# Optimization experiments

Hardware: AMD Instinct MI355X
Metric: run time of the kernel (lower is better)

## Reference

```python
import jax, jax.numpy as jnp
import numpy as np

B, T, C = 2, 2048, 1024
H = 16
HD = C // H  # 64


def setup_inputs() -> dict:
    key = jax.random.key(0)
    ks = jax.random.split(key, 6)
    s_in = 1.0 / np.sqrt(C)
    s_pr = 1.0 / np.sqrt(H * HD)
    x = jax.random.normal(ks[0], (B, T, C), dtype=jnp.float32)
    Wq = jax.random.uniform(ks[1], (H, C, HD), jnp.float32, -s_in, s_in)
    Wk = jax.random.uniform(ks[2], (H, C, HD), jnp.float32, -s_in, s_in)
    Wv = jax.random.uniform(ks[3], (H, C, HD), jnp.float32, -s_in, s_in)
    Wp = jax.random.uniform(ks[4], (H * HD, C), jnp.float32, -s_pr, s_pr)
    bp = jax.random.uniform(ks[5], (C,), jnp.float32, -s_pr, s_pr)
    return {"x": x, "Wq": Wq, "Wk": Wk, "Wv": Wv, "Wp": Wp, "bp": bp}


def reference(x, Wq, Wk, Wv, Wp, bp):
    # per-head projections: [B,T,C] x [H,C,D] -> [B,H,T,D]
    q = jnp.einsum('btc,hcd->bhtd', x, Wq)
    k = jnp.einsum('btc,hcd->bhtd', x, Wk)
    v = jnp.einsum('btc,hcd->bhtd', x, Wv)
    scale = HD ** (-0.5)
    scores = jnp.einsum('bhtd,bhsd->bhts', q, k) * scale  # [B,H,T,T]
    causal = jnp.tril(jnp.ones((T, T), dtype=bool))
    scores = jnp.where(causal, scores, -jnp.inf)
    w = jax.nn.softmax(scores, axis=-1)
    out = jnp.einsum('bhts,bhsd->bhtd', w, v)  # [B,H,T,D]
    # concat heads: [B,T,H*D] (head order matches torch.cat over heads)
    out = jnp.transpose(out, (0, 2, 1, 3)).reshape(B, T, H * HD)
    return out @ Wp + bp
```

## Files before the change

### kernel.cpp

```cpp
#include <hip/hip_runtime.h>
#include <hip/hip_bf16.h>
#include <hip/hip_cooperative_groups.h>

namespace cg = cooperative_groups;

#define B_NUM 2
#define T_SEQ 2048
#define C_DIM 1024
#define H_NUM 16
#define HD    64
#define M_TOT 4096
#define BH_N  32

typedef __attribute__((ext_vector_type(8))) short short8;
typedef __attribute__((ext_vector_type(4))) float floatx4;

__device__ __forceinline__ short f2bf(float f) {
    unsigned u = __float_as_uint(f);
    u += 0x7FFFu + ((u >> 16) & 1u);
    return (short)(u >> 16);
}

__device__ __forceinline__ unsigned pk2bf(float a, float b) {
    float2 f2; f2.x = a; f2.y = b;
    __hip_bfloat162 h = __float22bfloat162_rn(f2);
    unsigned u; __builtin_memcpy(&u, &h, 4); return u;
}

__device__ __forceinline__ void gld16(const short* g, short* l) {
    __builtin_amdgcn_global_load_lds(
        (const __attribute__((address_space(1))) void*)g,
        (__attribute__((address_space(3))) void*)l, 16, 0, 0);
}

__global__ __launch_bounds__(512, 2) void mega(
    const float* __restrict__ x,  const float* __restrict__ Wq,
    const float* __restrict__ Wk, const float* __restrict__ Wv,
    const float* __restrict__ Wp, const float* __restrict__ bp,
    short* __restrict__ xb, short* __restrict__ wt, short* __restrict__ wpt,
    short* __restrict__ qb, short* __restrict__ kb, short* __restrict__ vtb,
    short* __restrict__ attb, float* __restrict__ out) {

    __shared__ short smem[26112];
    cg::grid_group grid = cg::this_grid();

    const int G   = gridDim.x;
    const int bid = blockIdx.x;
    const int tid = threadIdx.x;
    const int lane = tid & 63, w = tid >> 6;
    const int hi = lane >> 4, llo = lane & 15;
    const int lrow = lane >> 3;
    const int lswz = ((lane & 7) ^ (lrow & 7)) * 8;
    const int fc0 = (hi ^ (llo & 7)) * 8;
    const int fc1 = ((hi + 4) ^ (llo & 7)) * 8;

    {
        int gtid = bid * 512 + tid;
        for (int i = gtid; i < 524288; i += G * 512) {
            int idx = i * 8;
            float4 a = *(const float4*)(x + idx);
            float4 b4 = *(const float4*)(x + idx + 4);
            short8 o;
            o[0] = f2bf(a.x);  o[1] = f2bf(a.y);  o[2] = f2bf(a.z);  o[3] = f2bf(a.w);
            o[4] = f2bf(b4.x); o[5] = f2bf(b4.y); o[6] = f2bf(b4.z); o[7] = f2bf(b4.w);
            *(short8*)(xb + idx) = o;
        }
        short (*sh)[72] = (short(*)[72])smem;
        for (int unit = bid; unit < 1024; unit += G) {
            __syncthreads();
            if (unit < 768) {
                const int y = unit >> 4, ct = unit & 15;
                const int which = y >> 4, h = y & 15;
                const float* W = ((which == 0) ? Wq : (which == 1) ? Wk : Wv)
                                 + (size_t)h * C_DIM * HD;
                const int c0 = ct * 64;
                #pragma unroll
                for (int p = 0; p < 2; ++p) {
                    int idx = tid + 512 * p;
                    int c = idx >> 4, d4 = idx & 15;
                    float4 v = *(const float4*)(W + (size_t)(c0 + c) * HD + d4 * 4);
                    sh[d4 * 4 + 0][c] = f2bf(v.x);
                    sh[d4 * 4 + 1][c] = f2bf(v.y);
                    sh[d4 * 4 + 2][c] = f2bf(v.z);
                    sh[d4 * 4 + 3][c] = f2bf(v.w);
                }
                __syncthreads();
                int d = tid >> 3, cc = tid & 7;
                short8 vv = *(const short8*)(&sh[d][cc * 8]);
                *(short8*)(wt + ((size_t)(which * 16 + h) * 64 + d) * C_DIM + c0 + cc * 8) = vv;
            } else {
                const int u2 = unit - 768;
                const int nt = u2 >> 4, ct = u2 & 15;
                #pragma unroll
                for (int p = 0; p < 2; ++p) {
                    int idx = tid + 512 * p;
                    int k = idx >> 4, n4 = idx & 15;
                    float4 v = *(const float4*)(Wp + (size_t)(ct * 64 + k) * C_DIM + nt * 64 + n4 * 4);
                    sh[n4 * 4 + 0][k] = f2bf(v.x);
                    sh[n4 * 4 + 1][k] = f2bf(v.y);
                    sh[n4 * 4 + 2][k] = f2bf(v.z);
                    sh[n4 * 4 + 3][k] = f2bf(v.w);
                }
                __syncthreads();
                int n = tid >> 3, cc = tid & 7;
                short8 vv = *(const short8*)(&sh[n][cc * 8]);
                *(short8*)(wpt + (size_t)(nt * 64 + n) * C_DIM + ct * 64 + cc * 8) = vv;
            }
        }
    }
    grid.sync();

    for (int tile = bid; tile < 512; tile += G) {
        const int mt = tile >> 4, ntg = tile & 15;
        const int m0 = mt * 128, n0 = ntg * 192;
        const int wm = w & 1, wn = w >> 1;
        short* As = smem;
        short* Bs = smem + 8192;

        floatx4 acc[4][3];
        #pragma unroll
        for (int i = 0; i < 4; ++i)
            #pragma unroll
            for (int j = 0; j < 3; ++j)
                #pragma unroll
                for (int r = 0; r < 4; ++r) acc[i][j][r] = 0.0f;

        const size_t a_base = (size_t)(m0 + w * 16 + lrow) * C_DIM + lswz;
        const size_t b_base = (size_t)(n0 + w * 24 + lrow) * C_DIM + lswz;

        for (int kt = 0; kt < C_DIM / 64; ++kt) {
            const int c0 = kt * 64;
            __syncthreads();
            #pragma unroll
            for (int p = 0; p < 2; ++p)
                gld16(xb + a_base + (size_t)p * 8 * C_DIM + c0, &As[(w * 16 + p * 8) * 64]);
            #pragma unroll
            for (int p = 0; p < 3; ++p)
                gld16(wt + b_base + (size_t)p * 8 * C_DIM + c0, &Bs[(w * 24 + p * 8) * 64]);
            __syncthreads();

            short8 af[4][2];
            #pragma unroll
            for (int mi = 0; mi < 4; ++mi) {
                const int row = wm * 64 + mi * 16 + llo;
                af[mi][0] = *(const short8*)(&As[row * 64 + fc0]);
                af[mi][1] = *(const short8*)(&As[row * 64 + fc1]);
            }
            #pragma unroll
            for (int ni = 0; ni < 3; ++ni) {
                const int row = wn * 48 + ni * 16 + llo;
                short8 b0 = *(const short8*)(&Bs[row * 64 + fc0]);
                short8 b1 = *(const short8*)(&Bs[row * 64 + fc1]);
                #pragma unroll
                for (int mi = 0; mi < 4; ++mi) {
                    acc[mi][ni] = __builtin_amdgcn_mfma_f32_16x16x32_bf16(af[mi][0], b0, acc[mi][ni], 0, 0, 0);
                    acc[mi][ni] = __builtin_amdgcn_mfma_f32_16x16x32_bf16(af[mi][1], b1, acc[mi][ni], 0, 0, 0);
                }
            }
        }

        const int bb = m0 >> 11;
        #pragma unroll
        for (int c = 0; c < 3; ++c) {
            const int n_chunk = n0 + 64 * c;
            const int which = n_chunk >> 10;
            const int h = (n_chunk >> 6) & 15;
            __syncthreads();
            if (which == 2) {
                short (*R)[136] = (short(*)[136])smem;
                #pragma unroll
                for (int ni = 0; ni < 3; ++ni) {
                    const int gcol = wn * 48 + ni * 16;
                    if ((gcol >> 6) == c) {
                        #pragma unroll
                        for (int mi = 0; mi < 4; ++mi)
                            #pragma unroll
                            for (int r = 0; r < 4; ++r)
                                R[(gcol & 63) + llo][wm * 64 + mi * 16 + hi * 4 + r] =
                                    f2bf(acc[mi][ni][r]);
                    }
                }
                __syncthreads();
                #pragma unroll
                for (int p = 0; p < 2; ++p) {
                    int idx = tid + 512 * p;
                    int rr = idx >> 4, cc = idx & 15;
                    short8 vv = *(const short8*)(&R[rr][cc * 8]);
                    int t = (m0 & 2047) + cc * 8;
                    *(short8*)(vtb + ((size_t)((bb * H_NUM + h) * HD + rr)) * T_SEQ + t) = vv;
                }
            } else {
                short (*R)[72] = (short(*)[72])smem;
                const float scl = (which == 0) ? 0.125f * 1.4426950408889634f : 1.0f;
                #pragma unroll
                for (int ni = 0; ni < 3; ++ni) {
                    const int gcol = wn * 48 + ni * 16;
                    if ((gcol >> 6) == c) {
                        #pragma unroll
                        for (int mi = 0; mi < 4; ++mi)
                            #pragma unroll
                            for (int r = 0; r < 4; ++r)
                                R[wm * 64 + mi * 16 + hi * 4 + r][(gcol & 63) + llo] =
                                    f2bf(acc[mi][ni][r] * scl);
                    }
                }
                __syncthreads();
                short* outp = (which == 0) ? qb : kb;
                #pragma unroll
                for (int p = 0; p < 2; ++p) {
                    int idx = tid + 512 * p;
                    int r = idx >> 3, cc = idx & 7;
                    short8 vv = *(const short8*)(&R[r][cc * 8]);
                    int t = (m0 + r) & 2047;
                    *(short8*)(outp + ((size_t)(bb * H_NUM + h) * T_SEQ + t) * HD + cc * 8) = vv;
                }
            }
        }
    }
    grid.sync();

    for (int unit = bid; unit < 512; unit += G) {
        const int bh = unit & 31;
        const int y = unit >> 5;
        const int qt = (y < 8) ? (15 - y) : (y - 8);
        const int b = bh >> 4, h = bh & 15;
        const short* K  = kb  + (size_t)bh * T_SEQ * HD;
        const short* Vt = vtb + (size_t)bh * HD * T_SEQ;

        short* Ks = smem;
        short* Vs = smem + 8192;
        short (*Ps)[76] = (short(*)[76])(smem + 16384);

        const int kmax = 2 * qt + 1;

        short8 qf[2];
        const int qcol0 = qt * 128 + w * 16;
        #pragma unroll
        for (int kh = 0; kh < 2; ++kh)
            qf[kh] = *(const short8*)(qb +
                ((size_t)bh * T_SEQ + qcol0 + llo) * HD + kh * 32 + hi * 8);

        short8 av4;
        #pragma unroll
        for (int j = 0; j < 8; ++j) av4[j] = (llo == 0) ? (short)0x3F80 : (short)0;

        gld16(K + (size_t)(w * 8 + lrow) * HD + lswz, &Ks[(w * 8) * 64]);
        gld16(Vt + (size_t)(w * 8 + lrow) * T_SEQ + lswz, &Vs[(w * 8) * 64]);

        floatx4 Oa[5];
        #pragma unroll
        for (int n = 0; n < 5; ++n)
            #pragma unroll
            for (int r = 0; r < 4; ++r) Oa[n][r] = 0.0f;

        for (int kt = 0; kt <= kmax; ++kt) {
            __syncthreads();
            const int buf = (kt & 1) * 4096;

            if (kt + 1 <= kmax) {
                const int s0 = (kt + 1) * 64;
                const int nb = ((kt + 1) & 1) * 4096;
                gld16(K + ((size_t)s0 + w * 8 + lrow) * HD + lswz, &Ks[nb + (w * 8) * 64]);
                gld16(Vt + (size_t)(w * 8 + lrow) * T_SEQ + s0 + lswz, &Vs[nb + (w * 8) * 64]);
            }

            short8 ak[4][2];
            #pragma unroll
            for (int nt = 0; nt < 4; ++nt) {
                const int row = nt * 16 + llo;
                ak[nt][0] = *(const short8*)(&Ks[buf + row * 64 + fc0]);
                ak[nt][1] = *(const short8*)(&Ks[buf + row * 64 + fc1]);
            }
            floatx4 sf[4];
            #pragma unroll
            for (int nt = 0; nt < 4; ++nt)
                #pragma unroll
                for (int r = 0; r < 4; ++r) sf[nt][r] = 0.0f;
            #pragma unroll
            for (int nt = 0; nt < 4; ++nt)
                #pragma unroll
                for (int kh = 0; kh < 2; ++kh)
                    sf[nt] = __builtin_amdgcn_mfma_f32_16x16x32_bf16(
                        ak[nt][kh], qf[kh], sf[nt], 0, 0, 0);

            const int sbase = kt * 64;
            if (sbase + 63 > qcol0) {
                const int qlane = qcol0 + llo;
                #pragma unroll
                for (int nt = 0; nt < 4; ++nt)
                    #pragma unroll
                    for (int r = 0; r < 4; ++r)
                        if (sbase + nt * 16 + hi * 4 + r > qlane) sf[nt][r] = -3.0e38f;
            }

            #pragma unroll
            for (int nt = 0; nt < 4; ++nt) {
                float p0 = __builtin_amdgcn_exp2f(sf[nt][0]);
                float p1 = __builtin_amdgcn_exp2f(sf[nt][1]);
                float p2 = __builtin_amdgcn_exp2f(sf[nt][2]);
                float p3 = __builtin_amdgcn_exp2f(sf[nt][3]);
                uint2 u; u.x = pk2bf(p0, p1); u.y = pk2bf(p2, p3);
                *(uint2*)(&Ps[w * 16 + llo][nt * 16 + hi * 4]) = u;
            }

            short8 av[5][2];
            #pragma unroll
            for (int nt2 = 0; nt2 < 4; ++nt2) {
                const int row = nt2 * 16 + llo;
                av[nt2][0] = *(const short8*)(&Vs[buf + row * 64 + fc0]);
                av[nt2][1] = *(const short8*)(&Vs[buf + row * 64 + fc1]);
            }
            av[4][0] = av4;
            av[4][1] = av4;
            short8 bpf[2];
            #pragma unroll
            for (int kh = 0; kh < 2; ++kh)
                bpf[kh] = *(const short8*)(&Ps[w * 16 + llo][kh * 32 + hi * 8]);
            #pragma unroll
            for (int nt2 = 0; nt2 < 5; ++nt2)
                #pragma unroll
                for (int kh = 0; kh < 2; ++kh)
                    Oa[nt2] = __builtin_amdgcn_mfma_f32_16x16x32_bf16(
                        av[nt2][kh], bpf[kh], Oa[nt2], 0, 0, 0);
        }

        {
            float lb = __shfl(Oa[4][0], llo);
            float inv = 1.0f / lb;
            #pragma unroll
            for (int nt2 = 0; nt2 < 4; ++nt2) {
                uint2 u;
                u.x = pk2bf(Oa[nt2][0] * inv, Oa[nt2][1] * inv);
                u.y = pk2bf(Oa[nt2][2] * inv, Oa[nt2][3] * inv);
                *(uint2*)(&Ps[w * 16 + llo][nt2 * 16 + hi * 4]) = u;
            }
        }
        __syncthreads();
        #pragma unroll
        for (int p = 0; p < 2; ++p) {
            int idx = tid + 512 * p;
            int r = idx >> 3, cc = idx & 7;
            short8 vv = *(const short8*)(&Ps[r][cc * 8]);
            *(short8*)(attb + ((size_t)(b * T_SEQ + qt * 128 + r)) * C_DIM + h * HD + cc * 8) = vv;
        }
        __syncthreads();
    }
    grid.sync();

    for (int tile = bid; tile < 512; tile += G) {
        const int mt = tile >> 4, ntg = tile & 15;
        const int m0 = mt * 128, n0 = ntg * 64;
        const int wm = w & 1, wn = w >> 1;
        short* As = smem;
        short* Bs = smem + 8192;

        floatx4 acc[4];
        #pragma unroll
        for (int i = 0; i < 4; ++i)
            #pragma unroll
            for (int r = 0; r < 4; ++r) acc[i][r] = 0.0f;

        const size_t a_base = (size_t)(m0 + w * 16 + lrow) * C_DIM + lswz;
        const size_t b_base = (size_t)(n0 + w * 8 + lrow) * C_DIM + lswz;

        for (int kt = 0; kt < C_DIM / 64; ++kt) {
            const int c0 = kt * 64;
            __syncthreads();
            #pragma unroll
            for (int p = 0; p < 2; ++p)
                gld16(attb + a_base + (size_t)p * 8 * C_DIM + c0, &As[(w * 16 + p * 8) * 64]);
            gld16(wpt + b_base + c0, &Bs[(w * 8) * 64]);
            __syncthreads();

            short8 af[4][2];
            #pragma unroll
            for (int mi = 0; mi < 4; ++mi) {
                const int row = wm * 64 + mi * 16 + llo;
                af[mi][0] = *(const short8*)(&As[row * 64 + fc0]);
                af[mi][1] = *(const short8*)(&As[row * 64 + fc1]);
            }
            const int brow = wn * 16 + llo;
            short8 b0 = *(const short8*)(&Bs[brow * 64 + fc0]);
            short8 b1 = *(const short8*)(&Bs[brow * 64 + fc1]);
            #pragma unroll
            for (int mi = 0; mi < 4; ++mi) {
                acc[mi] = __builtin_amdgcn_mfma_f32_16x16x32_bf16(af[mi][0], b0, acc[mi], 0, 0, 0);
                acc[mi] = __builtin_amdgcn_mfma_f32_16x16x32_bf16(af[mi][1], b1, acc[mi], 0, 0, 0);
            }
        }

        const int n = n0 + wn * 16 + llo;
        const float bias = bp[n];
        #pragma unroll
        for (int mi = 0; mi < 4; ++mi)
            #pragma unroll
            for (int r = 0; r < 4; ++r) {
                int m = m0 + wm * 64 + mi * 16 + hi * 4 + r;
                out[(size_t)m * C_DIM + n] = acc[mi][r] + bias;
            }
        __syncthreads();
    }
}

__global__ __launch_bounds__(256) void prep_k(
    const float* __restrict__ x, const float* __restrict__ Wq,
    const float* __restrict__ Wk, const float* __restrict__ Wv,
    const float* __restrict__ Wp,
    short* __restrict__ xb, short* __restrict__ wt, short* __restrict__ wpt) {
    const int bid = blockIdx.x;
    const int tid = threadIdx.x;
    if (bid < 2048) {
        int idx = (bid * 256 + tid) * 8;
        float4 a = *(const float4*)(x + idx);
        float4 b = *(const float4*)(x + idx + 4);
        short8 o;
        o[0] = f2bf(a.x); o[1] = f2bf(a.y); o[2] = f2bf(a.z); o[3] = f2bf(a.w);
        o[4] = f2bf(b.x); o[5] = f2bf(b.y); o[6] = f2bf(b.z); o[7] = f2bf(b.w);
        *(short8*)(xb + idx) = o;
        return;
    }
    const int b2 = bid - 2048;
    const int ct = b2 & 15, y = b2 >> 4;
    __shared__ short sh[64][72];
    if (y < 48) {
        const int which = y >> 4, h = y & 15;
        const float* W = ((which == 0) ? Wq : (which == 1) ? Wk : Wv) + (size_t)h * C_DIM * HD;
        const int c0 = ct * 64;
        #pragma unroll
        for (int p = 0; p < 4; ++p) {
            int idx = tid + 256 * p;
            int c = idx >> 4, d4 = idx & 15;
            float4 v = *(const float4*)(W + (size_t)(c0 + c) * HD + d4 * 4);
            sh[d4 * 4 + 0][c] = f2bf(v.x);
            sh[d4 * 4 + 1][c] = f2bf(v.y);
            sh[d4 * 4 + 2][c] = f2bf(v.z);
            sh[d4 * 4 + 3][c] = f2bf(v.w);
        }
        __syncthreads();
        #pragma unroll
        for (int p = 0; p < 2; ++p) {
            int idx = tid + 256 * p;
            int d = idx >> 3, cc = idx & 7;
            short8 vv = *(const short8*)(&sh[d][cc * 8]);
            *(short8*)(wt + ((size_t)(which * 16 + h) * 64 + d) * C_DIM + c0 + cc * 8) = vv;
        }
    } else {
        const int nt = y - 48;
        #pragma unroll
        for (int p = 0; p < 4; ++p) {
            int idx = tid + 256 * p;
            int k = idx >> 4, n4 = idx & 15;
            float4 v = *(const float4*)(Wp + (size_t)(ct * 64 + k) * C_DIM + nt * 64 + n4 * 4);
            sh[n4 * 4 + 0][k] = f2bf(v.x);
            sh[n4 * 4 + 1][k] = f2bf(v.y);
            sh[n4 * 4 + 2][k] = f2bf(v.z);
            sh[n4 * 4 + 3][k] = f2bf(v.w);
        }
        __syncthreads();
        #pragma unroll
        for (int p = 0; p < 2; ++p) {
            int idx = tid + 256 * p;
            int n = idx >> 3, cc = idx & 7;
            short8 vv = *(const short8*)(&sh[n][cc * 8]);
            *(short8*)(wpt + (size_t)(nt * 64 + n) * C_DIM + ct * 64 + cc * 8) = vv;
        }
    }
}

__global__ __launch_bounds__(256) void qkv_k(
    const short* __restrict__ xb, const short* __restrict__ wt,
    short* __restrict__ qb, short* __restrict__ kb, short* __restrict__ vtb) {
    const int mt = blockIdx.x, ntg = blockIdx.y;
    const int m0 = mt * 128, n0 = ntg * 128;
    const int which = ntg >> 3;
    const float sc = (which == 0) ? 0.125f * 1.4426950408889634f : 1.0f;

    __shared__ short smem[17408];
    short* As = smem;
    short* Bs = smem + 8192;

    const int tid = threadIdx.x;
    const int lane = tid & 63, w = tid >> 6;
    const int wm = w & 1, wn = w >> 1;
    const int hi = lane >> 4, llo = lane & 15;
    const int lrow = lane >> 3;
    const int lswz = ((lane & 7) ^ (lrow & 7)) * 8;
    const int fc0 = (hi ^ (llo & 7)) * 8;
    const int fc1 = ((hi + 4) ^ (llo & 7)) * 8;

    floatx4 acc[4][4];
    #pragma unroll
    for (int i = 0; i < 4; ++i)
        #pragma unroll
        for (int j = 0; j < 4; ++j)
            #pragma unroll
            for (int r = 0; r < 4; ++r) acc[i][j][r] = 0.0f;

    const size_t a_base = (size_t)(m0 + w * 32 + lrow) * C_DIM + lswz;
    const size_t b_base = (size_t)(n0 + w * 32 + lrow) * C_DIM + lswz;

    for (int kt = 0; kt < C_DIM / 64; ++kt) {
        const int c0 = kt * 64;
        __syncthreads();
        #pragma unroll
        for (int p = 0; p < 4; ++p) {
            gld16(xb + a_base + (size_t)p * 8 * C_DIM + c0, &As[(w * 32 + p * 8) * 64]);
            gld16(wt + b_base + (size_t)p * 8 * C_DIM + c0, &Bs[(w * 32 + p * 8) * 64]);
        }
        __syncthreads();

        short8 af[4][2];
        #pragma unroll
        for (int mi = 0; mi < 4; ++mi) {
            const int row = wm * 64 + mi * 16 + llo;
            af[mi][0] = *(const short8*)(&As[row * 64 + fc0]);
            af[mi][1] = *(const short8*)(&As[row * 64 + fc1]);
        }
        #pragma unroll
        for (int ni = 0; ni < 4; ++ni) {
            const int row = wn * 64 + ni * 16 + llo;
            short8 b0 = *(const short8*)(&Bs[row * 64 + fc0]);
            short8 b1 = *(const short8*)(&Bs[row * 64 + fc1]);
            #pragma unroll
            for (int mi = 0; mi < 4; ++mi) {
                acc[mi][ni] = __builtin_amdgcn_mfma_f32_16x16x32_bf16(af[mi][0], b0, acc[mi][ni], 0, 0, 0);
                acc[mi][ni] = __builtin_amdgcn_mfma_f32_16x16x32_bf16(af[mi][1], b1, acc[mi][ni], 0, 0, 0);
            }
        }
    }
    __syncthreads();

    short (*R)[136] = (short(*)[136])smem;
    if (which == 2) {
        #pragma unroll
        for (int mi = 0; mi < 4; ++mi)
            #pragma unroll
            for (int ni = 0; ni < 4; ++ni)
                #pragma unroll
                for (int r = 0; r < 4; ++r)
                    R[wn * 64 + ni * 16 + llo][wm * 64 + mi * 16 + hi * 4 + r] =
                        f2bf(acc[mi][ni][r]);
        __syncthreads();
        const int b = m0 >> 11;
        #pragma unroll
        for (int p = 0; p < 8; ++p) {
            int idx = tid + 256 * p;
            int rr = idx >> 4, cc = idx & 15;
            short8 vv = *(const short8*)(&R[rr][cc * 8]);
            int n = n0 + rr;
            int h = (n >> 6) & 15, d = n & 63;
            int t = (m0 & 2047) + cc * 8;
            *(short8*)(vtb + ((size_t)((b * H_NUM + h) * HD + d)) * T_SEQ + t) = vv;
        }
    } else {
        short* outp = (which == 0) ? qb : kb;
        #pragma unroll
        for (int mi = 0; mi < 4; ++mi)
            #pragma unroll
            for (int ni = 0; ni < 4; ++ni)
                #pragma unroll
                for (int r = 0; r < 4; ++r)
                    R[wm * 64 + mi * 16 + hi * 4 + r][wn * 64 + ni * 16 + llo] =
                        f2bf(acc[mi][ni][r] * sc);
        __syncthreads();
        #pragma unroll
        for (int p = 0; p < 8; ++p) {
            int idx = tid + 256 * p;
            int r = idx >> 4, cc = idx & 15;
            short8 vv = *(const short8*)(&R[r][cc * 8]);
            int mg = m0 + r;
            int b = mg >> 11, t = mg & 2047;
            int n = n0 + cc * 8;
            int h = (n >> 6) & 15, d = n & 63;
            *(short8*)(outp + ((size_t)(b * H_NUM + h) * T_SEQ + t) * HD + d) = vv;
        }
    }
}

__global__ __launch_bounds__(512) void attn_k(
    const short* __restrict__ qb, const short* __restrict__ kb,
    const short* __restrict__ vtb, short* __restrict__ attb) {
    const int bh = blockIdx.x;
    const int y = blockIdx.y;
    const int qt = (y < 8) ? (15 - y) : (y - 8);
    const int b = bh >> 4, h = bh & 15;
    const short* K  = kb  + (size_t)bh * T_SEQ * HD;
    const short* Vt = vtb + (size_t)bh * HD * T_SEQ;

    __shared__ short Ks[2][4096];
    __shared__ short Vs[2][4096];
    __shared__ short Ones[16 * 64];
    __shared__ short Ps[128][76];

    const int tid = threadIdx.x;
    const int lane = tid & 63, w = tid >> 6;
    const int hi = lane >> 4, llo = lane & 15;
    const int lrow = lane >> 3;
    const int lswz = ((lane & 7) ^ (lrow & 7)) * 8;
    const int fc0 = (hi ^ (llo & 7)) * 8;
    const int fc1 = ((hi + 4) ^ (llo & 7)) * 8;
    const int kmax = 2 * qt + 1;

    short8 qf[2];
    const int qcol0 = qt * 128 + w * 16;
    #pragma unroll
    for (int kh = 0; kh < 2; ++kh)
        qf[kh] = *(const short8*)(qb +
            ((size_t)bh * T_SEQ + qcol0 + llo) * HD + kh * 32 + hi * 8);

    for (int i = tid; i < 16 * 64; i += 512)
        Ones[i] = (i < 64) ? (short)0x3F80 : (short)0;

    gld16(K + (size_t)(w * 8 + lrow) * HD + lswz, &Ks[0][(w * 8) * 64]);
    gld16(Vt + (size_t)(w * 8 + lrow) * T_SEQ + lswz, &Vs[0][(w * 8) * 64]);

    floatx4 Oa[5];
    #pragma unroll
    for (int n = 0; n < 5; ++n)
        #pragma unroll
        for (int r = 0; r < 4; ++r) Oa[n][r] = 0.0f;

    for (int kt = 0; kt <= kmax; ++kt) {
        __syncthreads();
        const int buf = kt & 1;

        if (kt + 1 <= kmax) {
            const int s0 = (kt + 1) * 64;
            const int nb = buf ^ 1;
            gld16(K + ((size_t)s0 + w * 8 + lrow) * HD + lswz, &Ks[nb][(w * 8) * 64]);
            gld16(Vt + (size_t)(w * 8 + lrow) * T_SEQ + s0 + lswz, &Vs[nb][(w * 8) * 64]);
        }

        short8 ak[4][2];
        #pragma unroll
        for (int nt = 0; nt < 4; ++nt) {
            const int row = nt * 16 + llo;
            ak[nt][0] = *(const short8*)(&Ks[buf][row * 64 + fc0]);
            ak[nt][1] = *(const short8*)(&Ks[buf][row * 64 + fc1]);
        }
        floatx4 sf[4];
        #pragma unroll
        for (int nt = 0; nt < 4; ++nt)
            #pragma unroll
            for (int r = 0; r < 4; ++r) sf[nt][r] = 0.0f;
        #pragma unroll
        for (int nt = 0; nt < 4; ++nt)
            #pragma unroll
            for (int kh = 0; kh < 2; ++kh)
                sf[nt] = __builtin_amdgcn_mfma_f32_16x16x32_bf16(
                    ak[nt][kh], qf[kh], sf[nt], 0, 0, 0);

        const int sbase = kt * 64;
        if (sbase + 63 > qcol0) {
            const int qlane = qcol0 + llo;
            #pragma unroll
            for (int nt = 0; nt < 4; ++nt)
                #pragma unroll
                for (int r = 0; r < 4; ++r)
                    if (sbase + nt * 16 + hi * 4 + r > qlane) sf[nt][r] = -3.0e38f;
        }

        #pragma unroll
        for (int nt = 0; nt < 4; ++nt) {
            float p0 = __builtin_amdgcn_exp2f(sf[nt][0]);
            float p1 = __builtin_amdgcn_exp2f(sf[nt][1]);
            float p2 = __builtin_amdgcn_exp2f(sf[nt][2]);
            float p3 = __builtin_amdgcn_exp2f(sf[nt][3]);
            uint2 u; u.x = pk2bf(p0, p1); u.y = pk2bf(p2, p3);
            *(uint2*)(&Ps[w * 16 + llo][nt * 16 + hi * 4]) = u;
        }

        short8 av[5][2];
        #pragma unroll
        for (int nt2 = 0; nt2 < 4; ++nt2) {
            const int row = nt2 * 16 + llo;
            av[nt2][0] = *(const short8*)(&Vs[buf][row * 64 + fc0]);
            av[nt2][1] = *(const short8*)(&Vs[buf][row * 64 + fc1]);
        }
        av[4][0] = *(const short8*)(&Ones[llo * 64 + fc0]);
        av[4][1] = *(const short8*)(&Ones[llo * 64 + fc1]);
        short8 bpf[2];
        #pragma unroll
        for (int kh = 0; kh < 2; ++kh)
            bpf[kh] = *(const short8*)(&Ps[w * 16 + llo][kh * 32 + hi * 8]);
        #pragma unroll
        for (int nt2 = 0; nt2 < 5; ++nt2)
            #pragma unroll
            for (int kh = 0; kh < 2; ++kh)
                Oa[nt2] = __builtin_amdgcn_mfma_f32_16x16x32_bf16(
                    av[nt2][kh], bpf[kh], Oa[nt2], 0, 0, 0);
    }

    {
        float lb = __shfl(Oa[4][0], llo);
        float inv = 1.0f / lb;
        #pragma unroll
        for (int nt2 = 0; nt2 < 4; ++nt2) {
            uint2 u;
            u.x = pk2bf(Oa[nt2][0] * inv, Oa[nt2][1] * inv);
            u.y = pk2bf(Oa[nt2][2] * inv, Oa[nt2][3] * inv);
            *(uint2*)(&Ps[w * 16 + llo][nt2 * 16 + hi * 4]) = u;
        }
    }
    __syncthreads();
    #pragma unroll
    for (int p = 0; p < 2; ++p) {
        int idx = tid + 512 * p;
        int r = idx >> 3, cc = idx & 7;
        short8 vv = *(const short8*)(&Ps[r][cc * 8]);
        *(short8*)(attb + ((size_t)(b * T_SEQ + qt * 128 + r)) * C_DIM + h * HD + cc * 8) = vv;
    }
}

__global__ __launch_bounds__(256) void proj_k(
    const short* __restrict__ attb, const short* __restrict__ wpt,
    const float* __restrict__ bp, float* __restrict__ out) {
    const int mt = blockIdx.x, nt_g = blockIdx.y;
    const int m0 = mt * 128, n0 = nt_g * 64;

    __shared__ short As[8192];
    __shared__ short Bs[4096];

    const int tid = threadIdx.x;
    const int lane = tid & 63, w = tid >> 6;
    const int hi = lane >> 4, llo = lane & 15;
    const int lrow = lane >> 3;
    const int lswz = ((lane & 7) ^ (lrow & 7)) * 8;
    const int fc0 = (hi ^ (llo & 7)) * 8;
    const int fc1 = ((hi + 4) ^ (llo & 7)) * 8;

    floatx4 acc[2][4];
    #pragma unroll
    for (int i = 0; i < 2; ++i)
        #pragma unroll
        for (int j = 0; j < 4; ++j)
            #pragma unroll
            for (int r = 0; r < 4; ++r) acc[i][j][r] = 0.0f;

    const size_t a_base = (size_t)(m0 + w * 32 + lrow) * C_DIM + lswz;
    const size_t b_base = (size_t)(n0 + w * 16 + lrow) * C_DIM + lswz;

    for (int kt = 0; kt < C_DIM / 64; ++kt) {
        const int c0 = kt * 64;
        __syncthreads();
        #pragma unroll
        for (int p = 0; p < 4; ++p)
            gld16(attb + a_base + (size_t)p * 8 * C_DIM + c0, &As[(w * 32 + p * 8) * 64]);
        #pragma unroll
        for (int p = 0; p < 2; ++p)
            gld16(wpt + b_base + (size_t)p * 8 * C_DIM + c0, &Bs[(w * 16 + p * 8) * 64]);
        __syncthreads();

        short8 af[2][2];
        #pragma unroll
        for (int m2 = 0; m2 < 2; ++m2) {
            const int row = w * 32 + m2 * 16 + llo;
            af[m2][0] = *(const short8*)(&As[row * 64 + fc0]);
            af[m2][1] = *(const short8*)(&As[row * 64 + fc1]);
        }
        #pragma unroll
        for (int nt = 0; nt < 4; ++nt) {
            const int row = nt * 16 + llo;
            short8 b0 = *(const short8*)(&Bs[row * 64 + fc0]);
            short8 b1 = *(const short8*)(&Bs[row * 64 + fc1]);
            #pragma unroll
            for (int m2 = 0; m2 < 2; ++m2) {
                acc[m2][nt] = __builtin_amdgcn_mfma_f32_16x16x32_bf16(af[m2][0], b0, acc[m2][nt], 0, 0, 0);
                acc[m2][nt] = __builtin_amdgcn_mfma_f32_16x16x32_bf16(af[m2][1], b1, acc[m2][nt], 0, 0, 0);
            }
        }
    }

    #pragma unroll
    for (int nt = 0; nt < 4; ++nt) {
        const int n = n0 + nt * 16 + llo;
        const float bias = bp[n];
        #pragma unroll
        for (int m2 = 0; m2 < 2; ++m2)
            #pragma unroll
            for (int r = 0; r < 4; ++r) {
                int m = m0 + w * 32 + m2 * 16 + hi * 4 + r;
                out[(size_t)m * C_DIM + n] = acc[m2][nt][r] + bias;
            }
    }
}

extern "C" void kernel_launch(void* const* d_in, const int* in_sizes, int n_in,
                              void* d_out, int out_size, void* d_ws, size_t ws_size,
                              hipStream_t stream) {
    const float* x  = (const float*)d_in[0];
    const float* Wq = (const float*)d_in[1];
    const float* Wk = (const float*)d_in[2];
    const float* Wv = (const float*)d_in[3];
    const float* Wp = (const float*)d_in[4];
    const float* bp = (const float*)d_in[5];
    float* out = (float*)d_out;

    short* xb   = (short*)d_ws;
    short* wt   = xb  + (size_t)M_TOT * C_DIM;
    short* wpt  = wt  + (size_t)3 * H_NUM * HD * C_DIM;
    short* qb   = wpt + (size_t)C_DIM * C_DIM;
    short* kb   = qb  + (size_t)M_TOT * C_DIM;
    short* vtb  = kb  + (size_t)M_TOT * C_DIM;
    short* attb = vtb + (size_t)M_TOT * C_DIM;

    int maxBlk = 0;
    hipError_t qe = hipOccupancyMaxActiveBlocksPerMultiprocessor(&maxBlk, mega, 512, 0);
    int gridN = 256;
    if (qe == hipSuccess && maxBlk >= 2) gridN = 512;

    void* args[] = { (void*)&x, (void*)&Wq, (void*)&Wk, (void*)&Wv,
                     (void*)&Wp, (void*)&bp,
                     (void*)&xb, (void*)&wt, (void*)&wpt,
                     (void*)&qb, (void*)&kb, (void*)&vtb, (void*)&attb,
                     (void*)&out };
    hipError_t le = hipErrorUnknown;
    if (qe == hipSuccess && maxBlk >= 1)
        le = hipLaunchCooperativeKernel((void*)mega, dim3(gridN), dim3(512),
                                        args, 0, stream);
    if (le != hipSuccess) {
        (void)hipGetLastError();
        prep_k<<<dim3(3072), 256, 0, stream>>>(x, Wq, Wk, Wv, Wp, xb, wt, wpt);
        qkv_k <<<dim3(M_TOT / 128, 3 * C_DIM / 128), 256, 0, stream>>>(xb, wt, qb, kb, vtb);
        attn_k<<<dim3(BH_N, T_SEQ / 128), 512, 0, stream>>>(qb, kb, vtb, attb);
        proj_k<<<dim3(M_TOT / 128, C_DIM / 64), 256, 0, stream>>>(attb, wpt, bp, out);
    }
}
```

Before: 178.8 us.

## Replace cooperative mega-kernel with four separate kernel launches

Removes the single cooperative persistent kernel with grid-wide syncs and always launches separate prep, QKV, attention and projection kernels. Each stage can then use its own grid shape and occupancy instead of a fixed persistent grid, at the cost of extra launch overhead. The attention kernel also builds its ones-vector for the row-sum MFMA in registers instead of shared memory, and raises wave priority around the MFMA blocks.

```diff
diff --git a/kernel.cpp b/kernel.cpp
--- a/kernel.cpp
+++ b/kernel.cpp
@@ -1,8 +1,5 @@
 #include <hip/hip_runtime.h>
 #include <hip/hip_bf16.h>
-#include <hip/hip_cooperative_groups.h>
-
-namespace cg = cooperative_groups;
 
 #define B_NUM 2
 #define T_SEQ 2048
@@ -33,374 +30,6 @@
         (__attribute__((address_space(3))) void*)l, 16, 0, 0);
 }
 
-__global__ __launch_bounds__(512, 2) void mega(
-    const float* __restrict__ x,  const float* __restrict__ Wq,
-    const float* __restrict__ Wk, const float* __restrict__ Wv,
-    const float* __restrict__ Wp, const float* __restrict__ bp,
-    short* __restrict__ xb, short* __restrict__ wt, short* __restrict__ wpt,
-    short* __restrict__ qb, short* __restrict__ kb, short* __restrict__ vtb,
-    short* __restrict__ attb, float* __restrict__ out) {
-
-    __shared__ short smem[26112];
-    cg::grid_group grid = cg::this_grid();
-
-    const int G   = gridDim.x;
-    const int bid = blockIdx.x;
-    const int tid = threadIdx.x;
-    const int lane = tid & 63, w = tid >> 6;
-    const int hi = lane >> 4, llo = lane & 15;
-    const int lrow = lane >> 3;
-    const int lswz = ((lane & 7) ^ (lrow & 7)) * 8;
-    const int fc0 = (hi ^ (llo & 7)) * 8;
-    const int fc1 = ((hi + 4) ^ (llo & 7)) * 8;
-
-    {
-        int gtid = bid * 512 + tid;
-        for (int i = gtid; i < 524288; i += G * 512) {
-            int idx = i * 8;
-            float4 a = *(const float4*)(x + idx);
-            float4 b4 = *(const float4*)(x + idx + 4);
-            short8 o;
-            o[0] = f2bf(a.x);  o[1] = f2bf(a.y);  o[2] = f2bf(a.z);  o[3] = f2bf(a.w);
-            o[4] = f2bf(b4.x); o[5] = f2bf(b4.y); o[6] = f2bf(b4.z); o[7] = f2bf(b4.w);
-            *(short8*)(xb + idx) = o;
-        }
-        short (*sh)[72] = (short(*)[72])smem;
-        for (int unit = bid; unit < 1024; unit += G) {
-            __syncthreads();
-            if (unit < 768) {
-                const int y = unit >> 4, ct = unit & 15;
-                const int which = y >> 4, h = y & 15;
-                const float* W = ((which == 0) ? Wq : (which == 1) ? Wk : Wv)
-                                 + (size_t)h * C_DIM * HD;
-                const int c0 = ct * 64;
-                #pragma unroll
-                for (int p = 0; p < 2; ++p) {
-                    int idx = tid + 512 * p;
-                    int c = idx >> 4, d4 = idx & 15;
-                    float4 v = *(const float4*)(W + (size_t)(c0 + c) * HD + d4 * 4);
-                    sh[d4 * 4 + 0][c] = f2bf(v.x);
-                    sh[d4 * 4 + 1][c] = f2bf(v.y);
-                    sh[d4 * 4 + 2][c] = f2bf(v.z);
-                    sh[d4 * 4 + 3][c] = f2bf(v.w);
-                }
-                __syncthreads();
-                int d = tid >> 3, cc = tid & 7;
-                short8 vv = *(const short8*)(&sh[d][cc * 8]);
-                *(short8*)(wt + ((size_t)(which * 16 + h) * 64 + d) * C_DIM + c0 + cc * 8) = vv;
-            } else {
-                const int u2 = unit - 768;
-                const int nt = u2 >> 4, ct = u2 & 15;
-                #pragma unroll
-                for (int p = 0; p < 2; ++p) {
-                    int idx = tid + 512 * p;
-                    int k = idx >> 4, n4 = idx & 15;
-                    float4 v = *(const float4*)(Wp + (size_t)(ct * 64 + k) * C_DIM + nt * 64 + n4 * 4);
-                    sh[n4 * 4 + 0][k] = f2bf(v.x);
-                    sh[n4 * 4 + 1][k] = f2bf(v.y);
-                    sh[n4 * 4 + 2][k] = f2bf(v.z);
-                    sh[n4 * 4 + 3][k] = f2bf(v.w);
-                }
-                __syncthreads();
-                int n = tid >> 3, cc = tid & 7;
-                short8 vv = *(const short8*)(&sh[n][cc * 8]);
-                *(short8*)(wpt + (size_t)(nt * 64 + n) * C_DIM + ct * 64 + cc * 8) = vv;
-            }
-        }
-    }
-    grid.sync();
-
-    for (int tile = bid; tile < 512; tile += G) {
-        const int mt = tile >> 4, ntg = tile & 15;
-        const int m0 = mt * 128, n0 = ntg * 192;
-        const int wm = w & 1, wn = w >> 1;
-        short* As = smem;
-        short* Bs = smem + 8192;
-
-        floatx4 acc[4][3];
-        #pragma unroll
-        for (int i = 0; i < 4; ++i)
-            #pragma unroll
-            for (int j = 0; j < 3; ++j)
-                #pragma unroll
-                for (int r = 0; r < 4; ++r) acc[i][j][r] = 0.0f;
-
-        const size_t a_base = (size_t)(m0 + w * 16 + lrow) * C_DIM + lswz;
-        const size_t b_base = (size_t)(n0 + w * 24 + lrow) * C_DIM + lswz;
-
-        for (int kt = 0; kt < C_DIM / 64; ++kt) {
-            const int c0 = kt * 64;
-            __syncthreads();
-            #pragma unroll
-            for (int p = 0; p < 2; ++p)
-                gld16(xb + a_base + (size_t)p * 8 * C_DIM + c0, &As[(w * 16 + p * 8) * 64]);
-            #pragma unroll
-            for (int p = 0; p < 3; ++p)
-                gld16(wt + b_base + (size_t)p * 8 * C_DIM + c0, &Bs[(w * 24 + p * 8) * 64]);
-            __syncthreads();
-
-            short8 af[4][2];
-            #pragma unroll
-            for (int mi = 0; mi < 4; ++mi) {
-                const int row = wm * 64 + mi * 16 + llo;
-                af[mi][0] = *(const short8*)(&As[row * 64 + fc0]);
-                af[mi][1] = *(const short8*)(&As[row * 64 + fc1]);
-            }
-            #pragma unroll
-            for (int ni = 0; ni < 3; ++ni) {
-                const int row = wn * 48 + ni * 16 + llo;
-                short8 b0 = *(const short8*)(&Bs[row * 64 + fc0]);
-                short8 b1 = *(const short8*)(&Bs[row * 64 + fc1]);
-                #pragma unroll
-                for (int mi = 0; mi < 4; ++mi) {
-                    acc[mi][ni] = __builtin_amdgcn_mfma_f32_16x16x32_bf16(af[mi][0], b0, acc[mi][ni], 0, 0, 0);
-                    acc[mi][ni] = __builtin_amdgcn_mfma_f32_16x16x32_bf16(af[mi][1], b1, acc[mi][ni], 0, 0, 0);
-                }
-            }
-        }
-
-        const int bb = m0 >> 11;
-        #pragma unroll
-        for (int c = 0; c < 3; ++c) {
-            const int n_chunk = n0 + 64 * c;
-            const int which = n_chunk >> 10;
-            const int h = (n_chunk >> 6) & 15;
-            __syncthreads();
-            if (which == 2) {
-                short (*R)[136] = (short(*)[136])smem;
-                #pragma unroll
-                for (int ni = 0; ni < 3; ++ni) {
-                    const int gcol = wn * 48 + ni * 16;
-                    if ((gcol >> 6) == c) {
-                        #pragma unroll
-                        for (int mi = 0; mi < 4; ++mi)
-                            #pragma unroll
-                            for (int r = 0; r < 4; ++r)
-                                R[(gcol & 63) + llo][wm * 64 + mi * 16 + hi * 4 + r] =
-                                    f2bf(acc[mi][ni][r]);
-                    }
-                }
-                __syncthreads();
-                #pragma unroll
-                for (int p = 0; p < 2; ++p) {
-                    int idx = tid + 512 * p;
-                    int rr = idx >> 4, cc = idx & 15;
-                    short8 vv = *(const short8*)(&R[rr][cc * 8]);
-                    int t = (m0 & 2047) + cc * 8;
-                    *(short8*)(vtb + ((size_t)((bb * H_NUM + h) * HD + rr)) * T_SEQ + t) = vv;
-                }
-            } else {
-                short (*R)[72] = (short(*)[72])smem;
-                const float scl = (which == 0) ? 0.125f * 1.4426950408889634f : 1.0f;
-                #pragma unroll
-                for (int ni = 0; ni < 3; ++ni) {
-                    const int gcol = wn * 48 + ni * 16;
-                    if ((gcol >> 6) == c) {
-                        #pragma unroll
-                        for (int mi = 0; mi < 4; ++mi)
-                            #pragma unroll
-                            for (int r = 0; r < 4; ++r)
-                                R[wm * 64 + mi * 16 + hi * 4 + r][(gcol & 63) + llo] =
-                                    f2bf(acc[mi][ni][r] * scl);
-                    }
-                }
-                __syncthreads();
-                short* outp = (which == 0) ? qb : kb;
-                #pragma unroll
-                for (int p = 0; p < 2; ++p) {
-                    int idx = tid + 512 * p;
-                    int r = idx >> 3, cc = idx & 7;
-                    short8 vv = *(const short8*)(&R[r][cc * 8]);
-                    int t = (m0 + r) & 2047;
-                    *(short8*)(outp + ((size_t)(bb * H_NUM + h) * T_SEQ + t) * HD + cc * 8) = vv;
-                }
-            }
-        }
-    }
-    grid.sync();
-
-    for (int unit = bid; unit < 512; unit += G) {
-        const int bh = unit & 31;
-        const int y = unit >> 5;
-        const int qt = (y < 8) ? (15 - y) : (y - 8);
-        const int b = bh >> 4, h = bh & 15;
-        const short* K  = kb  + (size_t)bh * T_SEQ * HD;
-        const short* Vt = vtb + (size_t)bh * HD * T_SEQ;
-
-        short* Ks = smem;
-        short* Vs = smem + 8192;
-        short (*Ps)[76] = (short(*)[76])(smem + 16384);
-
-        const int kmax = 2 * qt + 1;
-
-        short8 qf[2];
-        const int qcol0 = qt * 128 + w * 16;
-        #pragma unroll
-        for (int kh = 0; kh < 2; ++kh)
-            qf[kh] = *(const short8*)(qb +
-                ((size_t)bh * T_SEQ + qcol0 + llo) * HD + kh * 32 + hi * 8);
-
-        short8 av4;
-        #pragma unroll
-        for (int j = 0; j < 8; ++j) av4[j] = (llo == 0) ? (short)0x3F80 : (short)0;
-
-        gld16(K + (size_t)(w * 8 + lrow) * HD + lswz, &Ks[(w * 8) * 64]);
-        gld16(Vt + (size_t)(w * 8 + lrow) * T_SEQ + lswz, &Vs[(w * 8) * 64]);
-
-        floatx4 Oa[5];
-        #pragma unroll
-        for (int n = 0; n < 5; ++n)
-            #pragma unroll
-            for (int r = 0; r < 4; ++r) Oa[n][r] = 0.0f;
-
-        for (int kt = 0; kt <= kmax; ++kt) {
-            __syncthreads();
-            const int buf = (kt & 1) * 4096;
-
-            if (kt + 1 <= kmax) {
-                const int s0 = (kt + 1) * 64;
-                const int nb = ((kt + 1) & 1) * 4096;
-                gld16(K + ((size_t)s0 + w * 8 + lrow) * HD + lswz, &Ks[nb + (w * 8) * 64]);
-                gld16(Vt + (size_t)(w * 8 + lrow) * T_SEQ + s0 + lswz, &Vs[nb + (w * 8) * 64]);
-            }
-
-            short8 ak[4][2];
-            #pragma unroll
-            for (int nt = 0; nt < 4; ++nt) {
-                const int row = nt * 16 + llo;
-                ak[nt][0] = *(const short8*)(&Ks[buf + row * 64 + fc0]);
-                ak[nt][1] = *(const short8*)(&Ks[buf + row * 64 + fc1]);
-            }
-            floatx4 sf[4];
-            #pragma unroll
-            for (int nt = 0; nt < 4; ++nt)
-                #pragma unroll
-                for (int r = 0; r < 4; ++r) sf[nt][r] = 0.0f;
-            #pragma unroll
-            for (int nt = 0; nt < 4; ++nt)
-                #pragma unroll
-                for (int kh = 0; kh < 2; ++kh)
-                    sf[nt] = __builtin_amdgcn_mfma_f32_16x16x32_bf16(
-                        ak[nt][kh], qf[kh], sf[nt], 0, 0, 0);
-
-            const int sbase = kt * 64;
-            if (sbase + 63 > qcol0) {
-                const int qlane = qcol0 + llo;
-                #pragma unroll
-                for (int nt = 0; nt < 4; ++nt)
-                    #pragma unroll
-                    for (int r = 0; r < 4; ++r)
-                        if (sbase + nt * 16 + hi * 4 + r > qlane) sf[nt][r] = -3.0e38f;
-            }
-
-            #pragma unroll
-            for (int nt = 0; nt < 4; ++nt) {
-                float p0 = __builtin_amdgcn_exp2f(sf[nt][0]);
-                float p1 = __builtin_amdgcn_exp2f(sf[nt][1]);
-                float p2 = __builtin_amdgcn_exp2f(sf[nt][2]);
-                float p3 = __builtin_amdgcn_exp2f(sf[nt][3]);
-                uint2 u; u.x = pk2bf(p0, p1); u.y = pk2bf(p2, p3);
-                *(uint2*)(&Ps[w * 16 + llo][nt * 16 + hi * 4]) = u;
-            }
-
-            short8 av[5][2];
-            #pragma unroll
-            for (int nt2 = 0; nt2 < 4; ++nt2) {
-                const int row = nt2 * 16 + llo;
-                av[nt2][0] = *(const short8*)(&Vs[buf + row * 64 + fc0]);
-                av[nt2][1] = *(const short8*)(&Vs[buf + row * 64 + fc1]);
-            }
-            av[4][0] = av4;
-            av[4][1] = av4;
-            short8 bpf[2];
-            #pragma unroll
-            for (int kh = 0; kh < 2; ++kh)
-                bpf[kh] = *(const short8*)(&Ps[w * 16 + llo][kh * 32 + hi * 8]);
-            #pragma unroll
-            for (int nt2 = 0; nt2 < 5; ++nt2)
-                #pragma unroll
-                for (int kh = 0; kh < 2; ++kh)
-                    Oa[nt2] = __builtin_amdgcn_mfma_f32_16x16x32_bf16(
-                        av[nt2][kh], bpf[kh], Oa[nt2], 0, 0, 0);
-        }
-
-        {
-            float lb = __shfl(Oa[4][0], llo);
-            float inv = 1.0f / lb;
-            #pragma unroll
-            for (int nt2 = 0; nt2 < 4; ++nt2) {
-                uint2 u;
-                u.x = pk2bf(Oa[nt2][0] * inv, Oa[nt2][1] * inv);
-                u.y = pk2bf(Oa[nt2][2] * inv, Oa[nt2][3] * inv);
-                *(uint2*)(&Ps[w * 16 + llo][nt2 * 16 + hi * 4]) = u;
-            }
-        }
-        __syncthreads();
-        #pragma unroll
-        for (int p = 0; p < 2; ++p) {
-            int idx = tid + 512 * p;
-            int r = idx >> 3, cc = idx & 7;
-            short8 vv = *(const short8*)(&Ps[r][cc * 8]);
-            *(short8*)(attb + ((size_t)(b * T_SEQ + qt * 128 + r)) * C_DIM + h * HD + cc * 8) = vv;
-        }
-        __syncthreads();
-    }
-    grid.sync();
-
-    for (int tile = bid; tile < 512; tile += G) {
-        const int mt = tile >> 4, ntg = tile & 15;
-        const int m0 = mt * 128, n0 = ntg * 64;
-        const int wm = w & 1, wn = w >> 1;
-        short* As = smem;
-        short* Bs = smem + 8192;
-
-        floatx4 acc[4];
-        #pragma unroll
-        for (int i = 0; i < 4; ++i)
-            #pragma unroll
-            for (int r = 0; r < 4; ++r) acc[i][r] = 0.0f;
-
-        const size_t a_base = (size_t)(m0 + w * 16 + lrow) * C_DIM + lswz;
-        const size_t b_base = (size_t)(n0 + w * 8 + lrow) * C_DIM + lswz;
-
-        for (int kt = 0; kt < C_DIM / 64; ++kt) {
-            const int c0 = kt * 64;
-            __syncthreads();
-            #pragma unroll
-            for (int p = 0; p < 2; ++p)
-                gld16(attb + a_base + (size_t)p * 8 * C_DIM + c0, &As[(w * 16 + p * 8) * 64]);
-            gld16(wpt + b_base + c0, &Bs[(w * 8) * 64]);
-            __syncthreads();
-
-            short8 af[4][2];
-            #pragma unroll
-            for (int mi = 0; mi < 4; ++mi) {
-                const int row = wm * 64 + mi * 16 + llo;
-                af[mi][0] = *(const short8*)(&As[row * 64 + fc0]);
-                af[mi][1] = *(const short8*)(&As[row * 64 + fc1]);
-            }
-            const int brow = wn * 16 + llo;
-            short8 b0 = *(const short8*)(&Bs[brow * 64 + fc0]);
-            short8 b1 = *(const short8*)(&Bs[brow * 64 + fc1]);
-            #pragma unroll
-            for (int mi = 0; mi < 4; ++mi) {
-                acc[mi] = __builtin_amdgcn_mfma_f32_16x16x32_bf16(af[mi][0], b0, acc[mi], 0, 0, 0);
-                acc[mi] = __builtin_amdgcn_mfma_f32_16x16x32_bf16(af[mi][1], b1, acc[mi], 0, 0, 0);
-            }
-        }
-
-        const int n = n0 + wn * 16 + llo;
-        const float bias = bp[n];
-        #pragma unroll
-        for (int mi = 0; mi < 4; ++mi)
-            #pragma unroll
-            for (int r = 0; r < 4; ++r) {
-                int m = m0 + wm * 64 + mi * 16 + hi * 4 + r;
-                out[(size_t)m * C_DIM + n] = acc[mi][r] + bias;
-            }
-        __syncthreads();
-    }
-}
 
 __global__ __launch_bounds__(256) void prep_k(
     const float* __restrict__ x, const float* __restrict__ Wq,
@@ -589,7 +218,6 @@
 
     __shared__ short Ks[2][4096];
     __shared__ short Vs[2][4096];
-    __shared__ short Ones[16 * 64];
     __shared__ short Ps[128][76];
 
     const int tid = threadIdx.x;
@@ -608,8 +236,9 @@
         qf[kh] = *(const short8*)(qb +
             ((size_t)bh * T_SEQ + qcol0 + llo) * HD + kh * 32 + hi * 8);
 
-    for (int i = tid; i < 16 * 64; i += 512)
-        Ones[i] = (i < 64) ? (short)0x3F80 : (short)0;
+    short8 av4;
+    #pragma unroll
+    for (int j = 0; j < 8; ++j) av4[j] = (llo == 0) ? (short)0x3F80 : (short)0;
 
     gld16(K + (size_t)(w * 8 + lrow) * HD + lswz, &Ks[0][(w * 8) * 64]);
     gld16(Vt + (size_t)(w * 8 + lrow) * T_SEQ + lswz, &Vs[0][(w * 8) * 64]);
@@ -643,12 +272,14 @@
         for (int nt = 0; nt < 4; ++nt)
             #pragma unroll
             for (int r = 0; r < 4; ++r) sf[nt][r] = 0.0f;
+        __builtin_amdgcn_s_setprio(1);
         #pragma unroll
         for (int nt = 0; nt < 4; ++nt)
             #pragma unroll
             for (int kh = 0; kh < 2; ++kh)
                 sf[nt] = __builtin_amdgcn_mfma_f32_16x16x32_bf16(
                     ak[nt][kh], qf[kh], sf[nt], 0, 0, 0);
+        __builtin_amdgcn_s_setprio(0);
 
         const int sbase = kt * 64;
         if (sbase + 63 > qcol0) {
@@ -677,18 +308,20 @@
             av[nt2][0] = *(const short8*)(&Vs[buf][row * 64 + fc0]);
             av[nt2][1] = *(const short8*)(&Vs[buf][row * 64 + fc1]);
         }
-        av[4][0] = *(const short8*)(&Ones[llo * 64 + fc0]);
-        av[4][1] = *(const short8*)(&Ones[llo * 64 + fc1]);
+        av[4][0] = av4;
+        av[4][1] = av4;
         short8 bpf[2];
         #pragma unroll
         for (int kh = 0; kh < 2; ++kh)
             bpf[kh] = *(const short8*)(&Ps[w * 16 + llo][kh * 32 + hi * 8]);
+        __builtin_amdgcn_s_setprio(1);
         #pragma unroll
         for (int nt2 = 0; nt2 < 5; ++nt2)
             #pragma unroll
             for (int kh = 0; kh < 2; ++kh)
                 Oa[nt2] = __builtin_amdgcn_mfma_f32_16x16x32_bf16(
                     av[nt2][kh], bpf[kh], Oa[nt2], 0, 0, 0);
+        __builtin_amdgcn_s_setprio(0);
     }
 
     {
@@ -804,25 +437,8 @@
     short* vtb  = kb  + (size_t)M_TOT * C_DIM;
     short* attb = vtb + (size_t)M_TOT * C_DIM;
 
-    int maxBlk = 0;
-    hipError_t qe = hipOccupancyMaxActiveBlocksPerMultiprocessor(&maxBlk, mega, 512, 0);
-    int gridN = 256;
-    if (qe == hipSuccess && maxBlk >= 2) gridN = 512;
-
-    void* args[] = { (void*)&x, (void*)&Wq, (void*)&Wk, (void*)&Wv,
-                     (void*)&Wp, (void*)&bp,
-                     (void*)&xb, (void*)&wt, (void*)&wpt,
-                     (void*)&qb, (void*)&kb, (void*)&vtb, (void*)&attb,
-                     (void*)&out };
-    hipError_t le = hipErrorUnknown;
-    if (qe == hipSuccess && maxBlk >= 1)
-        le = hipLaunchCooperativeKernel((void*)mega, dim3(gridN), dim3(512),
-                                        args, 0, stream);
-    if (le != hipSuccess) {
-        (void)hipGetLastError();
-        prep_k<<<dim3(3072), 256, 0, stream>>>(x, Wq, Wk, Wv, Wp, xb, wt, wpt);
-        qkv_k <<<dim3(M_TOT / 128, 3 * C_DIM / 128), 256, 0, stream>>>(xb, wt, qb, kb, vtb);
-        attn_k<<<dim3(BH_N, T_SEQ / 128), 512, 0, stream>>>(qb, kb, vtb, attb);
-        proj_k<<<dim3(M_TOT / 128, C_DIM / 64), 256, 0, stream>>>(attb, wpt, bp, out);
-    }
-}
+    prep_k<<<dim3(3072), 256, 0, stream>>>(x, Wq, Wk, Wv, Wp, xb, wt, wpt);
+    qkv_k <<<dim3(M_TOT / 128, 3 * C_DIM / 128), 256, 0, stream>>>(xb, wt, qb, kb, vtb);
+    attn_k<<<dim3(BH_N, T_SEQ / 128), 512, 0, stream>>>(qb, kb, vtb, attb);
+    proj_k<<<dim3(M_TOT / 128, C_DIM / 64), 256, 0, stream>>>(attb, wpt, bp, out);
+}
```

New measurement: 177.4 us. Within noise of the previous version (-0.8%).
